# Optimization experiments

Measured on AMD Instinct MI355X. Metric: run time of the kernel, lower is better.

## Reference

```python
import jax, jax.numpy as jnp
import numpy as np

S, B, D, O = 1024, 64, 1024, 512

def setup_inputs() -> dict:
    key = jax.random.key(0)
    k0, k1, k2, k3, k4, k5, k6, k7 = jax.random.split(key, 8)
    # ragged lengths in [S//2, S]; zero-pad x0 beyond each length
    lengths = jax.random.randint(k7, (B,), S // 2, S + 1)          # [B]
    mask = (jnp.arange(S)[:, None] < lengths[None, :]).astype(jnp.float32)  # [S,B]
    x0 = jax.random.normal(k0, (S, B, D), dtype=jnp.float32) * mask[:, :, None]
    x1 = mask[:, :, None]                                           # [S,B,1]
    s = 1.0 / np.sqrt(D)
    Wq = jax.random.normal(k1, (D, D), dtype=jnp.float32) * s
    bq = jax.random.normal(k2, (D,), dtype=jnp.float32) * s
    Wv = jax.random.normal(k3, (D, D), dtype=jnp.float32) * s
    bv = jax.random.normal(k4, (D,), dtype=jnp.float32) * s
    Wc = jax.random.normal(k5, (O, D), dtype=jnp.float32) * s
    bc = jax.random.normal(k6, (O,), dtype=jnp.float32) * s
    return {"x0": x0, "x1": x1, "Wq": Wq, "bq": bq, "Wv": Wv, "bv": bv, "Wc": Wc, "bc": bc}

def reference(x0, x1, Wq, bq, Wv, bv, Wc, bc):
    # x0: [S,B,D] zero-padded tokens; x1: [S,B,1] validity mask
    x_avg = jnp.sum(x0, axis=0) / jnp.sum(x1, axis=0)      # [B,D] masked mean
    q = x_avg @ Wq.T + bq                                   # [B,D]
    v = x0 @ Wv.T + bv                                      # [S,B,D]
    e = jnp.einsum('sbd,bd->sb', x0, q)                     # batched matvec scores
    e = jnp.where(e == 0, -jnp.inf, e)                      # zero-pad rows -> -inf
    a = jax.nn.softmax(e, axis=0)[:, :, None]               # [S,B,1], softmax over seq
    c = jnp.sum(a * v, axis=0)                              # [B,D] weighted pooling
    out = jax.nn.relu(c @ Wc.T + bc)                        # [B,O]
    return out, a
```

## Files before the change

### kernel.cpp

```cpp
#include <hip/hip_runtime.h>
#include <hip/hip_bf16.h>
#include <math.h>

#define S_ 1024
#define B_ 64
#define D_ 1024
#define O_ 512

typedef unsigned int uint_t;
typedef float f32x4 __attribute__((ext_vector_type(4)));

__device__ __forceinline__ float bflo(uint_t u){ return __uint_as_float(u << 16); }
__device__ __forceinline__ float bfhi(uint_t u){ return __uint_as_float(u & 0xffff0000u); }
__device__ __forceinline__ uint_t pack2(float lo, float hi){
  __hip_bfloat16 bl = __float2bfloat16(lo);
  __hip_bfloat16 bh = __float2bfloat16(hi);
  const unsigned short ul = *reinterpret_cast<unsigned short*>(&bl);
  const unsigned short uh = *reinterpret_cast<unsigned short*>(&bh);
  return (uint_t)ul | ((uint_t)uh << 16);
}

__global__ __launch_bounds__(256) void k_sum_cvt(const float* __restrict__ x0,
                                                 float* __restrict__ psum,
                                                 uint_t* __restrict__ xh){
  const int b = blockIdx.x, chunk = blockIdx.y, t = threadIdx.x;
  const int d8 = (t & 127) * 8;
  const int shalf = t >> 7;
  const size_t rowoff = (size_t)b*D_ + d8;
  f32x4 aLo = {0,0,0,0}, aHi = {0,0,0,0};
  const int s0 = chunk*64 + shalf*32;
  #pragma unroll 4
  for (int s = s0; s < s0+32; ++s){
    const float* p = x0 + (size_t)s*(B_*D_) + rowoff;
    const f32x4 vLo = __builtin_nontemporal_load((const f32x4*)p);
    const f32x4 vHi = __builtin_nontemporal_load((const f32x4*)(p+4));
    aLo += vLo; aHi += vHi;
    uint4 pk;
    pk.x = pack2(vLo.x, vLo.y); pk.y = pack2(vLo.z, vLo.w);
    pk.z = pack2(vHi.x, vHi.y); pk.w = pack2(vHi.z, vHi.w);
    *(uint4*)(xh + ((size_t)s*(B_*D_) + rowoff)/2) = pk;
  }
  __shared__ f32x4 lds[128][2];
  if (shalf){ lds[t & 127][0] = aLo; lds[t & 127][1] = aHi; }
  __syncthreads();
  if (!shalf){
    aLo += lds[t][0]; aHi += lds[t][1];
    float* dst = psum + ((size_t)chunk*B_ + b)*D_ + d8;
    *(f32x4*)dst = aLo;
    *(f32x4*)(dst+4) = aHi;
  }
}

__global__ __launch_bounds__(256) void k_reduce_cnt(const float* __restrict__ part,
                                                    const float* __restrict__ x1,
                                                    float* __restrict__ xsum,
                                                    float* __restrict__ invcnt){
  const int t = threadIdx.x;
  if (blockIdx.x >= 64){
    const int b = blockIdx.x - 64;
    float s = 0.f;
    #pragma unroll
    for (int k = 0; k < 4; ++k) s += x1[(size_t)(t + k*256)*B_ + b];
    for (int m = 32; m >= 1; m >>= 1) s += __shfl_xor(s, m, 64);
    __shared__ float red[4];
    if ((t & 63) == 0) red[t >> 6] = s;
    __syncthreads();
    if (t == 0) invcnt[b] = 1.0f / (red[0] + red[1] + red[2] + red[3]);
    return;
  }
  const size_t i = ((size_t)blockIdx.x*256 + t)*4;
  f32x4 a = *(const f32x4*)&part[i];
  #pragma unroll
  for (int c = 1; c < 16; ++c)
    a += *(const f32x4*)&part[(size_t)c*B_*D_ + i];
  *(f32x4*)&xsum[i] = a;
}

template<bool RELU>
__global__ __launch_bounds__(256) void k_gemm(const float* __restrict__ In,
                                              const float* __restrict__ W,
                                              const float* __restrict__ bias,
                                              const float* __restrict__ rowscale,
                                              float* __restrict__ Out, int M){
  __shared__ float sW[64][34];
  __shared__ float sIn[64][34];
  const int t = threadIdx.x;
  const int i0 = blockIdx.x * 32, b0 = blockIdx.y * 32;
  const int tx = t & 15, ty = t >> 4;
  float acc[2][2] = {{0.f,0.f},{0.f,0.f}};
  for (int k0 = 0; k0 < D_; k0 += 64){
    #pragma unroll
    for (int r = 0; r < 8; ++r){
      const int idx = t + r*256;
      const int kk = idx & 63, ii = idx >> 6;
      sW[kk][ii] = W[(size_t)(i0+ii)*D_ + k0 + kk];
    }
    #pragma unroll
    for (int r = 0; r < 8; ++r){
      const int idx = t + r*256;
      const int kk = idx & 63, bb = idx >> 6;
      float v = In[(size_t)(b0+bb)*D_ + k0 + kk];
      if (rowscale) v *= rowscale[b0+bb];
      sIn[kk][bb] = v;
    }
    __syncthreads();
    #pragma unroll
    for (int kk = 0; kk < 64; ++kk){
      const float2 w = *(const float2*)&sW[kk][ty*2];
      const float2 x = *(const float2*)&sIn[kk][tx*2];
      acc[0][0] += w.x*x.x; acc[0][1] += w.x*x.y;
      acc[1][0] += w.y*x.x; acc[1][1] += w.y*x.y;
    }
    __syncthreads();
  }
  #pragma unroll
  for (int a_ = 0; a_ < 2; ++a_)
    #pragma unroll
    for (int c_ = 0; c_ < 2; ++c_){
      const int i = i0 + ty*2 + a_, b = b0 + tx*2 + c_;
      float v = acc[a_][c_] + bias[i];
      if (RELU) v = fmaxf(v, 0.f);
      Out[(size_t)b*M + i] = v;
    }
}

__global__ __launch_bounds__(256) void k_dote(const uint_t* __restrict__ xh,
                                              const float* __restrict__ q,
                                              float* __restrict__ e){
  const int w = threadIdx.x >> 6, lane = threadIdx.x & 63;
  const int p = blockIdx.x*4 + w;
  const int b = p & (B_-1);
  const uint_t* row = xh + (size_t)p*(D_/2);
  const float* qr  = q + (size_t)b*D_;
  float acc = 0.f;
  #pragma unroll
  for (int it = 0; it < 2; ++it){
    const int e0 = lane*8 + it*512;
    const uint4  xv = *(const uint4*)&row[e0/2];
    const float4 q0 = *(const float4*)&qr[e0];
    const float4 q1 = *(const float4*)&qr[e0+4];
    acc += bflo(xv.x)*q0.x + bfhi(xv.x)*q0.y + bflo(xv.y)*q0.z + bfhi(xv.y)*q0.w
         + bflo(xv.z)*q1.x + bfhi(xv.z)*q1.y + bflo(xv.w)*q1.z + bfhi(xv.w)*q1.w;
  }
  for (int m = 32; m >= 1; m >>= 1) acc += __shfl_xor(acc, m, 64);
  if (lane == 0)
    e[p] = (acc == 0.0f) ? -__builtin_huge_valf() : acc;
}

__global__ __launch_bounds__(256) void k_wsum_sm(const uint_t* __restrict__ xh,
                                                 const float* __restrict__ e,
                                                 float* __restrict__ a_out,
                                                 float* __restrict__ y){
  const int b = blockIdx.x;
  const int d0u = blockIdx.y * 64;
  const int t = threadIdx.x;
  const int uidx = t & 63;
  const int soff = t >> 6;
  __shared__ float wbuf[S_];
  __shared__ float red[4];

  float v[4];
  #pragma unroll
  for (int k = 0; k < 4; ++k) v[k] = e[(size_t)(t + k*256)*B_ + b];
  float m = fmaxf(fmaxf(v[0],v[1]), fmaxf(v[2],v[3]));
  for (int msk = 32; msk >= 1; msk >>= 1) m = fmaxf(m, __shfl_xor(m, msk, 64));
  if ((t & 63) == 0) red[t >> 6] = m;
  __syncthreads();
  m = fmaxf(fmaxf(red[0],red[1]), fmaxf(red[2],red[3]));
  float ex[4]; float s = 0.f;
  #pragma unroll
  for (int k = 0; k < 4; ++k){ ex[k] = expf(v[k] - m); s += ex[k]; }
  for (int msk = 32; msk >= 1; msk >>= 1) s += __shfl_xor(s, msk, 64);
  __syncthreads();
  if ((t & 63) == 0) red[t >> 6] = s;
  __syncthreads();
  const float inv = 1.0f / (red[0] + red[1] + red[2] + red[3]);
  #pragma unroll
  for (int k = 0; k < 4; ++k){
    const float w = ex[k] * inv;
    wbuf[t + k*256] = w;
    if (blockIdx.y == 0) a_out[(size_t)(t + k*256)*B_ + b] = w;
  }
  __syncthreads();

  const size_t colbase = (size_t)b*(D_/2) + d0u + uidx;
  float2 acc0={0,0}, acc1={0,0}, acc2={0,0}, acc3={0,0};
  float2 acc4={0,0}, acc5={0,0}, acc6={0,0}, acc7={0,0};
  #pragma unroll 1
  for (int i = 0; i < 256; i += 8){
    const float w0 = wbuf[soff + (i+0)*4];
    const float w1 = wbuf[soff + (i+1)*4];
    const float w2 = wbuf[soff + (i+2)*4];
    const float w3 = wbuf[soff + (i+3)*4];
    const float w4 = wbuf[soff + (i+4)*4];
    const float w5 = wbuf[soff + (i+5)*4];
    const float w6 = wbuf[soff + (i+6)*4];
    const float w7 = wbuf[soff + (i+7)*4];
    const uint_t u0 = xh[(size_t)(soff + (i+0)*4)*(B_*D_/2) + colbase];
    const uint_t u1 = xh[(size_t)(soff + (i+1)*4)*(B_*D_/2) + colbase];
    const uint_t u2 = xh[(size_t)(soff + (i+2)*4)*(B_*D_/2) + colbase];
    const uint_t u3 = xh[(size_t)(soff + (i+3)*4)*(B_*D_/2) + colbase];
    const uint_t u4 = xh[(size_t)(soff + (i+4)*4)*(B_*D_/2) + colbase];
    const uint_t u5 = xh[(size_t)(soff + (i+5)*4)*(B_*D_/2) + colbase];
    const uint_t u6 = xh[(size_t)(soff + (i+6)*4)*(B_*D_/2) + colbase];
    const uint_t u7 = xh[(size_t)(soff + (i+7)*4)*(B_*D_/2) + colbase];
    acc0.x += w0*bflo(u0); acc0.y += w0*bfhi(u0);
    acc1.x += w1*bflo(u1); acc1.y += w1*bfhi(u1);
    acc2.x += w2*bflo(u2); acc2.y += w2*bfhi(u2);
    acc3.x += w3*bflo(u3); acc3.y += w3*bfhi(u3);
    acc4.x += w4*bflo(u4); acc4.y += w4*bfhi(u4);
    acc5.x += w5*bflo(u5); acc5.y += w5*bfhi(u5);
    acc6.x += w6*bflo(u6); acc6.y += w6*bfhi(u6);
    acc7.x += w7*bflo(u7); acc7.y += w7*bfhi(u7);
  }
  acc0.x += acc1.x; acc2.x += acc3.x; acc4.x += acc5.x; acc6.x += acc7.x;
  acc0.x += acc2.x; acc4.x += acc6.x; acc0.x += acc4.x;
  acc0.y += acc1.y; acc2.y += acc3.y; acc4.y += acc5.y; acc6.y += acc7.y;
  acc0.y += acc2.y; acc4.y += acc6.y; acc0.y += acc4.y;
  __shared__ float2 buf[4][64];
  buf[soff][uidx] = acc0;
  __syncthreads();
  if (soff == 0){
    float2 r = buf[0][uidx];
    r.x += buf[1][uidx].x + buf[2][uidx].x + buf[3][uidx].x;
    r.y += buf[1][uidx].y + buf[2][uidx].y + buf[3][uidx].y;
    ((float2*)y)[(size_t)b*(D_/2) + d0u + uidx] = r;
  }
}

extern "C" void kernel_launch(void* const* d_in, const int* in_sizes, int n_in,
                              void* d_out, int out_size, void* d_ws, size_t ws_size,
                              hipStream_t stream){
  const float* x0 = (const float*)d_in[0];
  const float* x1 = (const float*)d_in[1];
  const float* Wq = (const float*)d_in[2];
  const float* bq = (const float*)d_in[3];
  const float* Wv = (const float*)d_in[4];
  const float* bv = (const float*)d_in[5];
  const float* Wc = (const float*)d_in[6];
  const float* bc = (const float*)d_in[7];

  float* out_p = (float*)d_out;
  float* a_p   = out_p + (size_t)B_*O_;

  uint_t* xh  = (uint_t*)d_ws;
  float* fbase = (float*)((char*)d_ws + (size_t)S_*B_*(D_/2)*sizeof(uint_t));
  float* psum   = fbase;
  float* xsum   = fbase + (size_t)16*B_*D_;
  float* y      = fbase + (size_t)17*B_*D_;
  float* q      = fbase + (size_t)18*B_*D_;
  float* c      = fbase + (size_t)19*B_*D_;
  float* e      = fbase + (size_t)20*B_*D_;
  float* invcnt = fbase + (size_t)21*B_*D_;

  k_sum_cvt<<<dim3(B_, 16), 256, 0, stream>>>(x0, psum, xh);
  k_reduce_cnt<<<128, 256, 0, stream>>>(psum, x1, xsum, invcnt);
  k_gemm<false><<<dim3(D_/32, B_/32), 256, 0, stream>>>(xsum, Wq, bq, invcnt, q, D_);
  k_dote<<<(S_*B_)/4, 256, 0, stream>>>(xh, q, e);
  k_wsum_sm<<<dim3(B_, 8), 256, 0, stream>>>(xh, e, a_p, y);
  k_gemm<false><<<dim3(D_/32, B_/32), 256, 0, stream>>>(y, Wv, bv, nullptr, c, D_);
  k_gemm<true ><<<dim3(O_/32, B_/32), 256, 0, stream>>>(c, Wc, bc, nullptr, out_p, O_);
}
```

Before: 268.1 us.

## Split K across four thread groups inside GEMM blocks with shared-memory reduction

The small GEMM kernel now launches 1024 threads per block, and each 256-thread group processes a quarter of the K dimension into its own shared-memory tiles. Partial accumulators are written to shared memory and summed by the first group before bias and activation. This targets the low parallelism and long serial K loop of the tiny-grid GEMMs. The cost is larger shared-memory use, a final reduction pass, and lower per-block occupancy flexibility.

```diff
diff --git a/kernel.cpp b/kernel.cpp
--- a/kernel.cpp
+++ b/kernel.cpp
@@ -77,23 +77,25 @@
 }
 
 template<bool RELU>
-__global__ __launch_bounds__(256) void k_gemm(const float* __restrict__ In,
-                                              const float* __restrict__ W,
-                                              const float* __restrict__ bias,
-                                              const float* __restrict__ rowscale,
-                                              float* __restrict__ Out, int M){
-  __shared__ float sW[64][34];
-  __shared__ float sIn[64][34];
-  const int t = threadIdx.x;
+__global__ __launch_bounds__(1024) void k_gemm(const float* __restrict__ In,
+                                               const float* __restrict__ W,
+                                               const float* __restrict__ bias,
+                                               const float* __restrict__ rowscale,
+                                               float* __restrict__ Out, int M){
+  __shared__ float sW[4][64][34];
+  __shared__ float sIn[4][64][34];
+  const int t  = threadIdx.x & 255;
+  const int kg = threadIdx.x >> 8;
   const int i0 = blockIdx.x * 32, b0 = blockIdx.y * 32;
   const int tx = t & 15, ty = t >> 4;
   float acc[2][2] = {{0.f,0.f},{0.f,0.f}};
-  for (int k0 = 0; k0 < D_; k0 += 64){
+  const int kbase = kg*256;
+  for (int k0 = kbase; k0 < kbase+256; k0 += 64){
     #pragma unroll
     for (int r = 0; r < 8; ++r){
       const int idx = t + r*256;
       const int kk = idx & 63, ii = idx >> 6;
-      sW[kk][ii] = W[(size_t)(i0+ii)*D_ + k0 + kk];
+      sW[kg][kk][ii] = W[(size_t)(i0+ii)*D_ + k0 + kk];
     }
     #pragma unroll
     for (int r = 0; r < 8; ++r){
@@ -101,27 +103,38 @@
       const int kk = idx & 63, bb = idx >> 6;
       float v = In[(size_t)(b0+bb)*D_ + k0 + kk];
       if (rowscale) v *= rowscale[b0+bb];
-      sIn[kk][bb] = v;
+      sIn[kg][kk][bb] = v;
     }
     __syncthreads();
     #pragma unroll
     for (int kk = 0; kk < 64; ++kk){
-      const float2 w = *(const float2*)&sW[kk][ty*2];
-      const float2 x = *(const float2*)&sIn[kk][tx*2];
+      const float2 w = *(const float2*)&sW[kg][kk][ty*2];
+      const float2 x = *(const float2*)&sIn[kg][kk][tx*2];
       acc[0][0] += w.x*x.x; acc[0][1] += w.x*x.y;
       acc[1][0] += w.y*x.x; acc[1][1] += w.y*x.y;
     }
     __syncthreads();
   }
+  float* red = (float*)sW;
   #pragma unroll
   for (int a_ = 0; a_ < 2; ++a_)
     #pragma unroll
-    for (int c_ = 0; c_ < 2; ++c_){
-      const int i = i0 + ty*2 + a_, b = b0 + tx*2 + c_;
-      float v = acc[a_][c_] + bias[i];
-      if (RELU) v = fmaxf(v, 0.f);
-      Out[(size_t)b*M + i] = v;
-    }
+    for (int c_ = 0; c_ < 2; ++c_)
+      red[(kg*256 + t)*4 + a_*2 + c_] = acc[a_][c_];
+  __syncthreads();
+  if (kg == 0){
+    #pragma unroll
+    for (int a_ = 0; a_ < 2; ++a_)
+      #pragma unroll
+      for (int c_ = 0; c_ < 2; ++c_){
+        const int base = t*4 + a_*2 + c_;
+        float v = red[base] + red[1024+base] + red[2048+base] + red[3072+base];
+        const int i = i0 + ty*2 + a_, b = b0 + tx*2 + c_;
+        v += bias[i];
+        if (RELU) v = fmaxf(v, 0.f);
+        Out[(size_t)b*M + i] = v;
+      }
+  }
 }
 
 __global__ __launch_bounds__(256) void k_dote(const uint_t* __restrict__ xh,
@@ -255,9 +268,9 @@
 
   k_sum_cvt<<<dim3(B_, 16), 256, 0, stream>>>(x0, psum, xh);
   k_reduce_cnt<<<128, 256, 0, stream>>>(psum, x1, xsum, invcnt);
-  k_gemm<false><<<dim3(D_/32, B_/32), 256, 0, stream>>>(xsum, Wq, bq, invcnt, q, D_);
+  k_gemm<false><<<dim3(D_/32, B_/32), 1024, 0, stream>>>(xsum, Wq, bq, invcnt, q, D_);
   k_dote<<<(S_*B_)/4, 256, 0, stream>>>(xh, q, e);
   k_wsum_sm<<<dim3(B_, 8), 256, 0, stream>>>(xh, e, a_p, y);
-  k_gemm<false><<<dim3(D_/32, B_/32), 256, 0, stream>>>(y, Wv, bv, nullptr, c, D_);
-  k_gemm<true ><<<dim3(O_/32, B_/32), 256, 0, stream>>>(c, Wc, bc, nullptr, out_p, O_);
-}
+  k_gemm<false><<<dim3(D_/32, B_/32), 1024, 0, stream>>>(y, Wv, bv, nullptr, c, D_);
+  k_gemm<true ><<<dim3(O_/32, B_/32), 1024, 0, stream>>>(c, Wc, bc, nullptr, out_p, O_);
+}
```

New measurement: 215.0 us. -19.8%, faster.
